# Kernel optimization log

Measured on AMD Instinct MI355X. Metric: run time of the kernel, lower is better.

The kernel has to match this reference:

```python
import jax, jax.numpy as jnp
import numpy as np

N_NODES = 50000


def _gcn_edges(edge_index, n):
    # add self loops, then symmetric GCN normalization D^-1/2 (A+I) D^-1/2
    loop = jnp.arange(n, dtype=edge_index.dtype)
    src = jnp.concatenate([edge_index[0], loop])
    dst = jnp.concatenate([edge_index[1], loop])
    deg = jax.ops.segment_sum(jnp.ones_like(src, dtype=jnp.float32), dst, num_segments=n)
    dinv = jnp.where(deg > 0, jax.lax.rsqrt(deg), 0.0)
    norm = dinv[src] * dinv[dst]
    return src, dst, norm


def _encoder(x, edge_index, w1, b1, w2, b2, w3, b3, n):
    src, dst, norm = _gcn_edges(edge_index, n)

    def prop(h):
        # sparse spmm: scatter-add of normalized gathered source features
        return jax.ops.segment_sum(h[src] * norm[:, None], dst, num_segments=n)

    def layer(h, w, b):
        # powers [0,1,2]: incrementally apply adjacency, linear per power, concat
        outs, cur = [], h
        for p in range(w.shape[0]):
            if p > 0:
                cur = prop(cur)
            outs.append(cur @ w[p] + b[p])
        return jnp.tanh(jnp.concatenate(outs, axis=-1))

    h = layer(x, w1, b1)
    h = layer(h, w2, b2)
    return layer(h, w3, b3)


def setup_inputs() -> dict:
    key = jax.random.key(0)
    ks = jax.random.split(key, 16)
    n, e, d = N_NODES, 800000, 256
    inp = {
        "x": jax.random.normal(ks[0], (n, d), dtype=jnp.float32),
        "edge_index": jax.random.randint(ks[1], (2, e), 0, n, dtype=jnp.int64),
    }
    dims = [(d, 64), (192, 64), (192, 64)]
    i = 2
    for enc in ("out", "in"):
        for li, (din, dout) in enumerate(dims, start=1):
            s = 1.0 / np.sqrt(din)
            inp[f"w{enc}{li}"] = jax.random.uniform(ks[i], (3, din, dout), jnp.float32, -s, s); i += 1
            inp[f"b{enc}{li}"] = jax.random.uniform(ks[i], (3, dout), jnp.float32, -s, s); i += 1
    return inp


def reference(x, edge_index, wout1, bout1, wout2, bout2, wout3, bout3,
              win1, bin1, win2, bin2, win3, bin3):
    n = x.shape[0]
    zout = _encoder(x, edge_index, wout1, bout1, wout2, bout2, wout3, bout3, n)
    zin = _encoder(x, edge_index[::-1], win1, bin1, win2, bin2, win3, bin3, n)
    return (zout, zin)
```

## Files before the change

kernel.cpp:

```cpp
#include <hip/hip_runtime.h>
#include <hip/hip_bf16.h>

#define NN 50000
#define EE 800000
#define NTILES 782
#define NB 391

typedef __bf16 bf16x8 __attribute__((ext_vector_type(8)));
typedef unsigned short us8 __attribute__((ext_vector_type(8)));
typedef float f32x4 __attribute__((ext_vector_type(4)));

__device__ __forceinline__ unsigned short f2bf(float f) {
  unsigned u = __float_as_uint(f);
  u += 0x7FFFu + ((u >> 16) & 1u);
  return (unsigned short)(u >> 16);
}
__device__ __forceinline__ float bflo(unsigned u) { return __uint_as_float(u << 16); }
__device__ __forceinline__ float bfhi(unsigned u) { return __uint_as_float(u & 0xFFFF0000u); }
__device__ __forceinline__ float bf2f(unsigned short h) { return __uint_as_float(((unsigned)h) << 16); }
__device__ __forceinline__ float fast_tanh(float x) {
  float e = __expf(2.0f * x);
  return 1.0f - 2.0f / (e + 1.0f);
}


__global__ __launch_bounds__(256) void k_pack(const float* __restrict__ w0, const float* __restrict__ w1,
                                              const float* __restrict__ w2, const float* __restrict__ w3,
                                              const float* __restrict__ w4, const float* __restrict__ w5,
                                              unsigned short* t0, unsigned short* t1,
                                              unsigned short* t2, unsigned short* t3,
                                              unsigned short* t4, unsigned short* t5) {
  int y = blockIdx.y;
  const float* W = (y == 0) ? w0 : (y == 1) ? w1 : (y == 2) ? w2 : (y == 3) ? w3 : (y == 4) ? w4 : w5;
  unsigned short* T = (y == 0) ? t0 : (y == 1) ? t1 : (y == 2) ? t2 : (y == 3) ? t3 : (y == 4) ? t4 : t5;
  int K = (y < 2) ? 256 : 192;
  int tid = blockIdx.x * 256 + threadIdx.x;
  if (tid >= 192 * K) return;
  int col = tid / K;
  int k = tid - col * K;
  T[tid] = f2bf(W[(col >> 6) * (K * 64) + k * 64 + (col & 63)]);
}


__global__ __launch_bounds__(256) void k_hist(const int* __restrict__ ei, int* __restrict__ bCnt) {
  __shared__ int h[2 * NB];
  for (int i = threadIdx.x; i < 2 * NB; i += 256) h[i] = 0;
  __syncthreads();
  int base = blockIdx.x * 2048;
#pragma unroll
  for (int j = 0; j < 8; ++j) {
    int e = base + j * 256 + threadIdx.x;
    if (e < EE) {
      int s = ei[e], d = ei[EE + e];
      atomicAdd(&h[d >> 7], 1);
      atomicAdd(&h[NB + (s >> 7)], 1);
    }
  }
  __syncthreads();
  for (int i = threadIdx.x; i < 2 * NB; i += 256) {
    int c = h[i];
    if (c) atomicAdd(&bCnt[i], c);
  }
}

__global__ __launch_bounds__(512) void k_bscan(const int* __restrict__ bCnt,
                                               int* __restrict__ bOff, int* __restrict__ bCur) {
  __shared__ int sd[512];
  int z = blockIdx.x, t = threadIdx.x;
  sd[t] = (t < NB) ? bCnt[z * NB + t] : 0;
  __syncthreads();
  for (int o = 1; o < 512; o <<= 1) {
    int v = (t >= o) ? sd[t - o] : 0;
    __syncthreads();
    sd[t] += v;
    __syncthreads();
  }
  int ex = (t > 0) ? sd[t - 1] : 0;
  if (t < NB) { bOff[z * (NB + 1) + t] = ex; bCur[z * NB + t] = ex; }
  if (t == NB) bOff[z * (NB + 1) + NB] = ex;
}

__global__ __launch_bounds__(256) void k_scatter(const int* __restrict__ ei,
                                                 int* __restrict__ bCur,
                                                 unsigned* __restrict__ binA,
                                                 unsigned* __restrict__ binB) {
  __shared__ int h[2 * NB];
  for (int i = threadIdx.x; i < 2 * NB; i += 256) h[i] = 0;
  __syncthreads();
  int base = blockIdx.x * 2048;
  int s[8], d[8], la[8], lb[8];
#pragma unroll
  for (int j = 0; j < 8; ++j) {
    int e = base + j * 256 + threadIdx.x;
    d[j] = -1;
    if (e < EE) {
      s[j] = ei[e]; d[j] = ei[EE + e];
      la[j] = atomicAdd(&h[d[j] >> 7], 1);
      lb[j] = atomicAdd(&h[NB + (s[j] >> 7)], 1);
    }
  }
  __syncthreads();
  for (int i = threadIdx.x; i < 2 * NB; i += 256) {
    int c = h[i];
    if (c) h[i] = atomicAdd(&bCur[i], c);
  }
  __syncthreads();
#pragma unroll
  for (int j = 0; j < 8; ++j) {
    if (d[j] >= 0) {
      int pa = h[d[j] >> 7] + la[j];
      binA[pa] = ((unsigned)s[j] << 7) | (unsigned)(d[j] & 127);
      int pb = h[NB + (s[j] >> 7)] + lb[j];
      binB[pb] = ((unsigned)d[j] << 7) | (unsigned)(s[j] & 127);
    }
  }
}

__global__ __launch_bounds__(256) void k_build(const unsigned* __restrict__ binA,
                                               const unsigned* __restrict__ binB,
                                               const int* __restrict__ bOff,
                                               int* __restrict__ rpA, int* __restrict__ rpB,
                                               int* __restrict__ colA, int* __restrict__ colB,
                                               float* __restrict__ dinvA, float* __restrict__ dinvB) {
  int z = blockIdx.y, b = blockIdx.x, t = threadIdx.x;
  const unsigned* bin = z ? binB : binA;
  int* rp = z ? rpB : rpA;
  int* col = z ? colB : colA;
  float* dinv = z ? dinvB : dinvA;

  int e0 = bOff[z * (NB + 1) + b], e1 = bOff[z * (NB + 1) + b + 1];

  __shared__ int cnt[128];
  __shared__ int scn[128];
  __shared__ int cur[128];
  if (t < 128) cnt[t] = 0;
  __syncthreads();
  for (int e = e0 + t; e < e1; e += 256) atomicAdd(&cnt[bin[e] & 127], 1);
  __syncthreads();
  if (t < 128) scn[t] = cnt[t];
  __syncthreads();
  for (int o = 1; o < 128; o <<= 1) {
    int v = (t < 128 && t >= o) ? scn[t - o] : 0;
    __syncthreads();
    if (t < 128) scn[t] += v;
    __syncthreads();
  }
  if (t < 128) {
    int ex = scn[t] - cnt[t];
    cur[t] = ex;
    int node = b * 128 + t;
    if (node <= NN) rp[node] = e0 + ex;
    if (node < NN) dinv[node] = rsqrtf((float)(cnt[t] + 1));
  }
  if (b == 0 && t < 16) col[EE + t] = 0;
  __syncthreads();
  for (int e = e0 + t; e < e1; e += 256) {
    unsigned p = bin[e];
    int pos = e0 + atomicAdd(&cur[p & 127], 1);
    col[pos] = (int)(p >> 7);
  }
}


template<int K, bool F32IN>
__global__ __launch_bounds__(256) void k_gemm(const void* __restrict__ in0, const void* __restrict__ in1,
                                              const unsigned short* __restrict__ Wt0,
                                              const unsigned short* __restrict__ Wt1,
                                              const float* __restrict__ dinvA, const float* __restrict__ dinvB,
                                              unsigned short* __restrict__ Z0, unsigned short* __restrict__ Z1) {
  constexpr int KS = K / 32;
  constexpr int KP = K + 8;
  __shared__ unsigned short A_lds[64 * KP];
  __shared__ float dvt[64];

  int z = blockIdx.y;
  const void* Ain = z ? in1 : in0;
  const unsigned short* Wt = z ? Wt1 : Wt0;
  const float* dinv = z ? dinvB : dinvA;
  unsigned short* Zo = z ? Z1 : Z0;

  int t = threadIdx.x;
  int lane = t & 63, wv = t >> 6;
  int nloc = lane & 15, quad = lane >> 4;

  bf16x8 b[3][KS];
#pragma unroll
  for (int nt = 0; nt < 3; ++nt) {
    int ncol = wv * 48 + nt * 16 + nloc;
#pragma unroll
    for (int ks = 0; ks < KS; ++ks)
      b[nt][ks] = *(const bf16x8*)(Wt + (size_t)ncol * K + ks * 32 + quad * 8);
  }

  for (int bm = blockIdx.x; bm < NTILES; bm += gridDim.x) {
    int m0 = bm * 64;
    __syncthreads();
    if (t < 64) dvt[t] = (m0 + t < NN) ? dinv[m0 + t] : 0.f;
#pragma unroll
    for (int it = 0; it < KS; ++it) {
      int c = it * 256 + t;
      int row = c / (K / 8);
      int kc  = c % (K / 8);
      int gr = m0 + row;
      us8 val;
      if (F32IN) {
        float4 v0 = make_float4(0, 0, 0, 0), v1 = make_float4(0, 0, 0, 0);
        if (gr < NN) {
          const float* Af = (const float*)Ain + (size_t)gr * K + kc * 8;
          v0 = *(const float4*)(Af);
          v1 = *(const float4*)(Af + 4);
        }
        val[0] = f2bf(v0.x); val[1] = f2bf(v0.y); val[2] = f2bf(v0.z); val[3] = f2bf(v0.w);
        val[4] = f2bf(v1.x); val[5] = f2bf(v1.y); val[6] = f2bf(v1.z); val[7] = f2bf(v1.w);
      } else {
        if (gr < NN) val = *(const us8*)((const unsigned short*)Ain + (size_t)gr * K + kc * 8);
        else         val = (us8)0;
      }
      *(us8*)(&A_lds[row * KP + kc * 8]) = val;
    }
    __syncthreads();

    f32x4 acc[4][3];
#pragma unroll
    for (int mt = 0; mt < 4; ++mt)
#pragma unroll
      for (int nt = 0; nt < 3; ++nt) acc[mt][nt] = (f32x4){0.f, 0.f, 0.f, 0.f};

#pragma unroll
    for (int ks = 0; ks < KS; ++ks) {
      bf16x8 a[4];
#pragma unroll
      for (int mt = 0; mt < 4; ++mt)
        a[mt] = *(const bf16x8*)(&A_lds[(mt * 16 + nloc) * KP + ks * 32 + quad * 8]);
#pragma unroll
      for (int mt = 0; mt < 4; ++mt)
#pragma unroll
        for (int nt = 0; nt < 3; ++nt)
          acc[mt][nt] = __builtin_amdgcn_mfma_f32_16x16x32_bf16(a[mt], b[nt][ks], acc[mt][nt], 0, 0, 0);
    }

#pragma unroll
    for (int mt = 0; mt < 4; ++mt) {
      int rowb = m0 + mt * 16 + quad * 4;
#pragma unroll
      for (int nt = 0; nt < 3; ++nt) {
        int colg = wv * 48 + nt * 16 + nloc;
        bool sc = (wv * 48 + nt * 16) >= 64;
#pragma unroll
        for (int r = 0; r < 4; ++r) {
          int rr = rowb + r;
          float scale = sc ? dvt[mt * 16 + quad * 4 + r] : 1.0f;
          if (rr < NN) Zo[(size_t)rr * 192 + colg] = f2bf(acc[mt][nt][r] * scale);
        }
      }
    }
  }
}


__global__ __launch_bounds__(256) void k_prop1(const unsigned short* __restrict__ Z0,
                                               const unsigned short* __restrict__ Z1,
                                               unsigned short* __restrict__ T0,
                                               unsigned short* __restrict__ T1,
                                               const int* __restrict__ rpA, const int* __restrict__ rpB,
                                               const int* __restrict__ colA, const int* __restrict__ colB,
                                               const float* __restrict__ dinvA, const float* __restrict__ dinvB) {
  int z = blockIdx.y;
  const unsigned short* Z = z ? Z1 : Z0;
  unsigned short* T = z ? T1 : T0;
  const int* rp = z ? rpB : rpA;
  const int* col = z ? colB : colA;
  const float* dinv = z ? dinvB : dinvA;

  int wv = threadIdx.x >> 6, lane = threadIdx.x & 63;
  int h = lane >> 5, l = lane & 31;
  int v = __builtin_amdgcn_readfirstlane(blockIdx.x * 4 + wv);

  int e0 = rp[v], e1 = rp[v + 1];
  float dv = dinv[v];

  float a0 = 0, a1 = 0, a2 = 0, a3 = 0;

  int e = e0;
  if (e + 16 <= e1) {
    int idx[8];
#pragma unroll
    for (int j = 0; j < 8; ++j) idx[j] = col[e + 2 * j + h];
    e += 16;
    while (e + 16 <= e1) {
      int nidx[8];
#pragma unroll
      for (int j = 0; j < 8; ++j) nidx[j] = col[e + 2 * j + h];
      uint2 pp[8];
#pragma unroll
      for (int j = 0; j < 8; ++j) pp[j] = *(const uint2*)(Z + (size_t)idx[j] * 192 + 64 + l * 4);
#pragma unroll
      for (int j = 0; j < 8; ++j) {
        a0 += bflo(pp[j].x); a1 += bfhi(pp[j].x);
        a2 += bflo(pp[j].y); a3 += bfhi(pp[j].y);
      }
#pragma unroll
      for (int j = 0; j < 8; ++j) idx[j] = nidx[j];
      e += 16;
    }
    uint2 pp[8];
#pragma unroll
    for (int j = 0; j < 8; ++j) pp[j] = *(const uint2*)(Z + (size_t)idx[j] * 192 + 64 + l * 4);
#pragma unroll
    for (int j = 0; j < 8; ++j) {
      a0 += bflo(pp[j].x); a1 += bfhi(pp[j].x);
      a2 += bflo(pp[j].y); a3 += bfhi(pp[j].y);
    }
  }
  int r = e1 - e;
  if (r > 0) {
    int idx[8];
#pragma unroll
    for (int j = 0; j < 8; ++j) idx[j] = col[e + 2 * j + h];
    uint2 pp[8];
#pragma unroll
    for (int j = 0; j < 8; ++j) pp[j] = *(const uint2*)(Z + (size_t)idx[j] * 192 + 64 + l * 4);
#pragma unroll
    for (int j = 0; j < 8; ++j) if (2 * j + h < r) {
      a0 += bflo(pp[j].x); a1 += bfhi(pp[j].x);
      a2 += bflo(pp[j].y); a3 += bfhi(pp[j].y);
    }
  }

  a0 += __shfl_xor(a0, 32); a1 += __shfl_xor(a1, 32);
  a2 += __shfl_xor(a2, 32); a3 += __shfl_xor(a3, 32);

  uint2 sv = *(const uint2*)(Z + (size_t)v * 192 + 64 + l * 4);
  a0 += bflo(sv.x); a1 += bfhi(sv.x); a2 += bflo(sv.y); a3 += bfhi(sv.y);

  float sc = dv * (l >= 16 ? dv : 1.0f);
  if (h == 0) {
    uint2 o;
    o.x = (unsigned)f2bf(a0 * sc) | ((unsigned)f2bf(a1 * sc) << 16);
    o.y = (unsigned)f2bf(a2 * sc) | ((unsigned)f2bf(a3 * sc) << 16);
    *(uint2*)(T + (size_t)v * 128 + l * 4) = o;
  }
}


template<bool FINAL>
__global__ __launch_bounds__(256) void k_combine(const unsigned short* __restrict__ Z0,
                                                 const unsigned short* __restrict__ Z1,
                                                 const unsigned short* __restrict__ T0,
                                                 const unsigned short* __restrict__ T1,
                                                 unsigned short* __restrict__ H0,
                                                 unsigned short* __restrict__ H1,
                                                 float* __restrict__ out,
                                                 const float* __restrict__ bia0, const float* __restrict__ bia1,
                                                 const int* __restrict__ rpA, const int* __restrict__ rpB,
                                                 const int* __restrict__ colA, const int* __restrict__ colB,
                                                 const float* __restrict__ dinvA, const float* __restrict__ dinvB) {
  int z = blockIdx.y;
  const unsigned short* Z = z ? Z1 : Z0;
  const unsigned short* T = z ? T1 : T0;
  unsigned short* H = z ? H1 : H0;
  const float* bias = z ? bia1 : bia0;
  const int* rp = z ? rpB : rpA;
  const int* col = z ? colB : colA;
  const float* dinv = z ? dinvB : dinvA;

  int wv = threadIdx.x >> 6, lane = threadIdx.x & 63;
  int h = lane >> 5, l = lane & 31;
  int v = __builtin_amdgcn_readfirstlane(blockIdx.x * 4 + wv);

  int e0 = rp[v], e1 = rp[v + 1];
  float dv = dinv[v];

  float u0 = 0, u1 = 0;

  int e = e0;
  if (e + 16 <= e1) {
    int idx[8];
#pragma unroll
    for (int j = 0; j < 8; ++j) idx[j] = col[e + 2 * j + h];
    e += 16;
    while (e + 16 <= e1) {
      int nidx[8];
#pragma unroll
      for (int j = 0; j < 8; ++j) nidx[j] = col[e + 2 * j + h];
      unsigned pp[8];
#pragma unroll
      for (int j = 0; j < 8; ++j) pp[j] = *(const unsigned*)(T + (size_t)idx[j] * 128 + 64 + l * 2);
#pragma unroll
      for (int j = 0; j < 8; ++j) { u0 += bflo(pp[j]); u1 += bfhi(pp[j]); }
#pragma unroll
      for (int j = 0; j < 8; ++j) idx[j] = nidx[j];
      e += 16;
    }
    unsigned pp[8];
#pragma unroll
    for (int j = 0; j < 8; ++j) pp[j] = *(const unsigned*)(T + (size_t)idx[j] * 128 + 64 + l * 2);
#pragma unroll
    for (int j = 0; j < 8; ++j) { u0 += bflo(pp[j]); u1 += bfhi(pp[j]); }
  }
  int r = e1 - e;
  if (r > 0) {
    int idx[8];
#pragma unroll
    for (int j = 0; j < 8; ++j) idx[j] = col[e + 2 * j + h];
    unsigned pp[8];
#pragma unroll
    for (int j = 0; j < 8; ++j) pp[j] = *(const unsigned*)(T + (size_t)idx[j] * 128 + 64 + l * 2);
#pragma unroll
    for (int j = 0; j < 8; ++j) if (2 * j + h < r) { u0 += bflo(pp[j]); u1 += bfhi(pp[j]); }
  }

  u0 += __shfl_xor(u0, 32);
  u1 += __shfl_xor(u1, 32);
  float ua = __shfl(u0, lane >> 1);
  float ub = __shfl(u1, lane >> 1);
  float u = (lane & 1) ? ub : ua;

  const unsigned short* Trow = T + (size_t)v * 128;
  u += bf2f(Trow[64 + lane]);
  u *= dv;

  float p0 = fast_tanh(bf2f(Z[(size_t)v * 192 + lane]) + bias[lane]);
  float p1 = fast_tanh(bf2f(Trow[lane]) + bias[64 + lane]);
  float p2 = fast_tanh(u + bias[128 + lane]);

  if (FINAL) {
    float* o = out + (size_t)z * NN * 192 + (size_t)v * 192;
    o[lane] = p0; o[lane + 64] = p1; o[lane + 128] = p2;
  } else {
    unsigned short* hh = H + (size_t)v * 192;
    hh[lane] = f2bf(p0); hh[lane + 64] = f2bf(p1); hh[lane + 128] = f2bf(p2);
  }
}


extern "C" void kernel_launch(void* const* d_in, const int* in_sizes, int n_in,
                              void* d_out, int out_size, void* d_ws, size_t ws_size,
                              hipStream_t stream) {
  const float* x  = (const float*)d_in[0];
  const int* ei   = (const int*)d_in[1];
  const float* wout1 = (const float*)d_in[2];
  const float* bout1 = (const float*)d_in[3];
  const float* wout2 = (const float*)d_in[4];
  const float* bout2 = (const float*)d_in[5];
  const float* wout3 = (const float*)d_in[6];
  const float* bout3 = (const float*)d_in[7];
  const float* win1  = (const float*)d_in[8];
  const float* bin1  = (const float*)d_in[9];
  const float* win2  = (const float*)d_in[10];
  const float* bin2  = (const float*)d_in[11];
  const float* win3  = (const float*)d_in[12];
  const float* bin3  = (const float*)d_in[13];
  float* out = (float*)d_out;

  char* p = (char*)d_ws;
  auto alloc = [&](size_t bytes) { char* r = p; p += (bytes + 255) & ~(size_t)255; return r; };
  int* rpA   = (int*)alloc((size_t)(NN + 1) * 4);
  int* rpB   = (int*)alloc((size_t)(NN + 1) * 4);
  int* colA  = (int*)alloc((size_t)(EE + 16) * 4);
  int* colB  = (int*)alloc((size_t)(EE + 16) * 4);
  float* dinvA = (float*)alloc((size_t)NN * 4);
  float* dinvB = (float*)alloc((size_t)NN * 4);
  int* bCnt  = (int*)alloc((size_t)2 * NB * 4);
  int* bOff  = (int*)alloc((size_t)2 * (NB + 1) * 4);
  int* bCur  = (int*)alloc((size_t)2 * NB * 4);
  unsigned short* wt0 = (unsigned short*)alloc((size_t)192 * 256 * 2);
  unsigned short* wt1 = (unsigned short*)alloc((size_t)192 * 256 * 2);
  unsigned short* wt2 = (unsigned short*)alloc((size_t)192 * 192 * 2);
  unsigned short* wt3 = (unsigned short*)alloc((size_t)192 * 192 * 2);
  unsigned short* wt4 = (unsigned short*)alloc((size_t)192 * 192 * 2);
  unsigned short* wt5 = (unsigned short*)alloc((size_t)192 * 192 * 2);
  unsigned short* Z0 = (unsigned short*)alloc((size_t)NN * 192 * 2);
  unsigned short* Z1 = (unsigned short*)alloc((size_t)NN * 192 * 2);
  unsigned short* T0 = (unsigned short*)alloc((size_t)NN * 128 * 2);
  unsigned short* T1 = (unsigned short*)alloc((size_t)NN * 128 * 2);
  unsigned short* H0 = (unsigned short*)alloc((size_t)NN * 192 * 2);
  unsigned short* H1 = (unsigned short*)alloc((size_t)NN * 192 * 2);

  unsigned* binA = (unsigned*)Z0;
  unsigned* binB = (unsigned*)Z1;

  k_pack<<<dim3(192, 6), 256, 0, stream>>>(wout1, win1, wout2, win2, wout3, win3,
                                           wt0, wt1, wt2, wt3, wt4, wt5);
  hipMemsetAsync(bCnt, 0, (size_t)2 * NB * 4, stream);
  k_hist<<<391, 256, 0, stream>>>(ei, bCnt);
  k_bscan<<<2, 512, 0, stream>>>(bCnt, bOff, bCur);
  k_scatter<<<391, 256, 0, stream>>>(ei, bCur, binA, binB);
  k_build<<<dim3(NB, 2), 256, 0, stream>>>(binA, binB, bOff, rpA, rpB, colA, colB, dinvA, dinvB);

  dim3 gGemm(391, 2);
  dim3 gProp(12500, 2);

  k_gemm<256, true><<<gGemm, 256, 0, stream>>>(x, x, wt0, wt1, dinvA, dinvB, Z0, Z1);
  k_prop1<<<gProp, 256, 0, stream>>>(Z0, Z1, T0, T1, rpA, rpB, colA, colB, dinvA, dinvB);
  k_combine<false><<<gProp, 256, 0, stream>>>(Z0, Z1, T0, T1, H0, H1, nullptr, bout1, bin1,
                                              rpA, rpB, colA, colB, dinvA, dinvB);
  k_gemm<192, false><<<gGemm, 256, 0, stream>>>(H0, H1, wt2, wt3, dinvA, dinvB, Z0, Z1);
  k_prop1<<<gProp, 256, 0, stream>>>(Z0, Z1, T0, T1, rpA, rpB, colA, colB, dinvA, dinvB);
  k_combine<false><<<gProp, 256, 0, stream>>>(Z0, Z1, T0, T1, H0, H1, nullptr, bout2, bin2,
                                              rpA, rpB, colA, colB, dinvA, dinvB);
  k_gemm<192, false><<<gGemm, 256, 0, stream>>>(H0, H1, wt4, wt5, dinvA, dinvB, Z0, Z1);
  k_prop1<<<gProp, 256, 0, stream>>>(Z0, Z1, T0, T1, rpA, rpB, colA, colB, dinvA, dinvB);
  k_combine<true><<<gProp, 256, 0, stream>>>(Z0, Z1, T0, T1, H0, H1, out, bout3, bin3,
                                             rpA, rpB, colA, colB, dinvA, dinvB);
}
```

Measured before the change: 590.7 us.

## Load GEMM A tiles directly to LDS with XOR swizzle and pre-cast x to bf16

Adds a kernel that casts x to bf16 once into a padded buffer, so the first GEMM is no longer read as fp32 and converted twice (once per direction). The GEMM A-tile load now uses global_load_lds 16-byte direct-to-LDS transfers with an XOR swizzle in place of the padded layout, avoiding the register round trip and bank conflicts. The GEMM grid is halved, giving each block more tiles over which to reuse its register-resident weights. This needs padded H/X buffers so the last tile reads in bounds, and relies on the swizzle being consistent between the store and the MFMA operand reads.

New measurement: 574.0 us. 2.8% less time.

```diff
diff --git a/kernel.cpp b/kernel.cpp
--- a/kernel.cpp
+++ b/kernel.cpp
@@ -2,6 +2,7 @@
 #include <hip/hip_bf16.h>
 
 #define NN 50000
+#define MPAD 50048
 #define EE 800000
 #define NTILES 782
 #define NB 391
@@ -21,6 +22,29 @@
 __device__ __forceinline__ float fast_tanh(float x) {
   float e = __expf(2.0f * x);
   return 1.0f - 2.0f / (e + 1.0f);
+}
+
+__device__ __forceinline__ void gload_lds16(const unsigned short* g, unsigned short* l) {
+  __builtin_amdgcn_global_load_lds(
+      (const __attribute__((address_space(1))) unsigned*)g,
+      (__attribute__((address_space(3))) unsigned*)l, 16, 0, 0);
+}
+
+
+__global__ __launch_bounds__(256) void k_xcast(const float* __restrict__ x, unsigned short* __restrict__ Xb) {
+  int c = blockIdx.x * 256 + threadIdx.x;
+  size_t base = (size_t)c * 8;
+  us8 v;
+  if (base < (size_t)NN * 256) {
+    const float* xp = x + base;
+    float4 v0 = *(const float4*)xp;
+    float4 v1 = *(const float4*)(xp + 4);
+    v[0] = f2bf(v0.x); v[1] = f2bf(v0.y); v[2] = f2bf(v0.z); v[3] = f2bf(v0.w);
+    v[4] = f2bf(v1.x); v[5] = f2bf(v1.y); v[6] = f2bf(v1.z); v[7] = f2bf(v1.w);
+  } else {
+    v = (us8)0;
+  }
+  *(us8*)(Xb + base) = v;
 }
 
 
@@ -162,19 +186,20 @@
 }
 
 
-template<int K, bool F32IN>
-__global__ __launch_bounds__(256) void k_gemm(const void* __restrict__ in0, const void* __restrict__ in1,
+template<int K>
+__global__ __launch_bounds__(256) void k_gemm(const unsigned short* __restrict__ in0,
+                                              const unsigned short* __restrict__ in1,
                                               const unsigned short* __restrict__ Wt0,
                                               const unsigned short* __restrict__ Wt1,
                                               const float* __restrict__ dinvA, const float* __restrict__ dinvB,
                                               unsigned short* __restrict__ Z0, unsigned short* __restrict__ Z1) {
+  constexpr int KC = K / 8;
   constexpr int KS = K / 32;
-  constexpr int KP = K + 8;
-  __shared__ unsigned short A_lds[64 * KP];
+  __shared__ unsigned short A_lds[64 * K];
   __shared__ float dvt[64];
 
   int z = blockIdx.y;
-  const void* Ain = z ? in1 : in0;
+  const unsigned short* Ain = z ? in1 : in0;
   const unsigned short* Wt = z ? Wt1 : Wt0;
   const float* dinv = z ? dinvB : dinvA;
   unsigned short* Zo = z ? Z1 : Z0;
@@ -197,26 +222,12 @@
     __syncthreads();
     if (t < 64) dvt[t] = (m0 + t < NN) ? dinv[m0 + t] : 0.f;
 #pragma unroll
-    for (int it = 0; it < KS; ++it) {
-      int c = it * 256 + t;
-      int row = c / (K / 8);
-      int kc  = c % (K / 8);
-      int gr = m0 + row;
-      us8 val;
-      if (F32IN) {
-        float4 v0 = make_float4(0, 0, 0, 0), v1 = make_float4(0, 0, 0, 0);
-        if (gr < NN) {
-          const float* Af = (const float*)Ain + (size_t)gr * K + kc * 8;
-          v0 = *(const float4*)(Af);
-          v1 = *(const float4*)(Af + 4);
-        }
-        val[0] = f2bf(v0.x); val[1] = f2bf(v0.y); val[2] = f2bf(v0.z); val[3] = f2bf(v0.w);
-        val[4] = f2bf(v1.x); val[5] = f2bf(v1.y); val[6] = f2bf(v1.z); val[7] = f2bf(v1.w);
-      } else {
-        if (gr < NN) val = *(const us8*)((const unsigned short*)Ain + (size_t)gr * K + kc * 8);
-        else         val = (us8)0;
-      }
-      *(us8*)(&A_lds[row * KP + kc * 8]) = val;
+    for (int it = 0; it < KC / 4; ++it) {
+      int s = it * 256 + t;
+      int row = s / KC;
+      int kc_sw = s - row * KC;
+      int kc_g = kc_sw ^ (row & 7);
+      gload_lds16(Ain + (size_t)(m0 + row) * K + kc_g * 8, &A_lds[s * 8]);
     }
     __syncthreads();
 
@@ -230,8 +241,11 @@
     for (int ks = 0; ks < KS; ++ks) {
       bf16x8 a[4];
 #pragma unroll
-      for (int mt = 0; mt < 4; ++mt)
-        a[mt] = *(const bf16x8*)(&A_lds[(mt * 16 + nloc) * KP + ks * 32 + quad * 8]);
+      for (int mt = 0; mt < 4; ++mt) {
+        int r = mt * 16 + nloc;
+        int kc = (ks * 4 + quad) ^ (r & 7);
+        a[mt] = *(const bf16x8*)(&A_lds[r * K + kc * 8]);
+      }
 #pragma unroll
       for (int mt = 0; mt < 4; ++mt)
 #pragma unroll
@@ -470,36 +484,38 @@
   unsigned short* wt3 = (unsigned short*)alloc((size_t)192 * 192 * 2);
   unsigned short* wt4 = (unsigned short*)alloc((size_t)192 * 192 * 2);
   unsigned short* wt5 = (unsigned short*)alloc((size_t)192 * 192 * 2);
+  unsigned short* Xb = (unsigned short*)alloc((size_t)MPAD * 256 * 2);
   unsigned short* Z0 = (unsigned short*)alloc((size_t)NN * 192 * 2);
   unsigned short* Z1 = (unsigned short*)alloc((size_t)NN * 192 * 2);
   unsigned short* T0 = (unsigned short*)alloc((size_t)NN * 128 * 2);
   unsigned short* T1 = (unsigned short*)alloc((size_t)NN * 128 * 2);
-  unsigned short* H0 = (unsigned short*)alloc((size_t)NN * 192 * 2);
-  unsigned short* H1 = (unsigned short*)alloc((size_t)NN * 192 * 2);
+  unsigned short* H0 = (unsigned short*)alloc((size_t)MPAD * 192 * 2);
+  unsigned short* H1 = (unsigned short*)alloc((size_t)MPAD * 192 * 2);
 
   unsigned* binA = (unsigned*)Z0;
   unsigned* binB = (unsigned*)Z1;
 
   k_pack<<<dim3(192, 6), 256, 0, stream>>>(wout1, win1, wout2, win2, wout3, win3,
                                            wt0, wt1, wt2, wt3, wt4, wt5);
+  k_xcast<<<MPAD / 8, 256, 0, stream>>>(x, Xb);
   hipMemsetAsync(bCnt, 0, (size_t)2 * NB * 4, stream);
   k_hist<<<391, 256, 0, stream>>>(ei, bCnt);
   k_bscan<<<2, 512, 0, stream>>>(bCnt, bOff, bCur);
   k_scatter<<<391, 256, 0, stream>>>(ei, bCur, binA, binB);
   k_build<<<dim3(NB, 2), 256, 0, stream>>>(binA, binB, bOff, rpA, rpB, colA, colB, dinvA, dinvB);
 
-  dim3 gGemm(391, 2);
+  dim3 gGemm(196, 2);
   dim3 gProp(12500, 2);
 
-  k_gemm<256, true><<<gGemm, 256, 0, stream>>>(x, x, wt0, wt1, dinvA, dinvB, Z0, Z1);
+  k_gemm<256><<<gGemm, 256, 0, stream>>>(Xb, Xb, wt0, wt1, dinvA, dinvB, Z0, Z1);
   k_prop1<<<gProp, 256, 0, stream>>>(Z0, Z1, T0, T1, rpA, rpB, colA, colB, dinvA, dinvB);
   k_combine<false><<<gProp, 256, 0, stream>>>(Z0, Z1, T0, T1, H0, H1, nullptr, bout1, bin1,
                                               rpA, rpB, colA, colB, dinvA, dinvB);
-  k_gemm<192, false><<<gGemm, 256, 0, stream>>>(H0, H1, wt2, wt3, dinvA, dinvB, Z0, Z1);
+  k_gemm<192><<<gGemm, 256, 0, stream>>>(H0, H1, wt2, wt3, dinvA, dinvB, Z0, Z1);
   k_prop1<<<gProp, 256, 0, stream>>>(Z0, Z1, T0, T1, rpA, rpB, colA, colB, dinvA, dinvB);
   k_combine<false><<<gProp, 256, 0, stream>>>(Z0, Z1, T0, T1, H0, H1, nullptr, bout2, bin2,
                                               rpA, rpB, colA, colB, dinvA, dinvB);
-  k_gemm<192, false><<<gGemm, 256, 0, stream>>>(H0, H1, wt4, wt5, dinvA, dinvB, Z0, Z1);
+  k_gemm<192><<<gGemm, 256, 0, stream>>>(H0, H1, wt4, wt5, dinvA, dinvB, Z0, Z1);
   k_prop1<<<gProp, 256, 0, stream>>>(Z0, Z1, T0, T1, rpA, rpB, colA, colB, dinvA, dinvB);
   k_combine<true><<<gProp, 256, 0, stream>>>(Z0, Z1, T0, T1, H0, H1, out, bout3, bin3,
                                              rpA, rpB, colA, colB, dinvA, dinvB);
```
